# Kernel optimization log

Hardware: AMD Instinct MI355X
Metric: run time of the kernel (lower is better)

The kernel has to match this reference:

```python
import jax, jax.numpy as jnp
import numpy as np

B = 256      # batch
N_SRC = 10   # number of (x, y, mass) triplets per sample -> coord_v has 3*N_SRC cols
NMC = 16     # mass-channel bins
LL = 128     # spatial grid size


def setup_inputs() -> dict:
    key = jax.random.key(0)
    k1, = jax.random.split(key, 1)
    u = jax.random.uniform(k1, (B, 3 * N_SRC), dtype=jnp.float32)
    cols = jnp.arange(3 * N_SRC)
    is_mass = (cols % 3) == 2
    # x,y uniform in [0,1); mass = 10**(3u) in [1,1000) so log10(mass)/3 in [0,1)
    coord_v = jnp.where(is_mass, 10.0 ** (u * 3.0), u)
    lows = jnp.array([0.0, 0.0, 0.0], dtype=jnp.float32)
    highs = jnp.array([1.0, 1.0, 3.0], dtype=jnp.float32)
    return {"coord_v": coord_v, "lows": lows, "highs": highs, "nmc": NMC, "L": LL}


def reference(coord_v, lows, highs, nmc, L):
    n_batch, n_cols = coord_v.shape
    n = n_cols // 3  # number of triplets per sample

    # v_to_grid: log10 the mass columns, then normalize by tiled lows/highs
    v10 = coord_v.at[:, 2::3].set(jnp.log10(coord_v[:, 2::3]))
    lo = jnp.tile(lows, n)   # [3n]
    hi = jnp.tile(highs, n)  # [3n]
    coord_grid = (v10 - lo) / (hi - lo)  # [B, 3n]

    tr = coord_grid.reshape(-1, 3)  # [B*n, 3] rows of (x, y, m)
    x_i = jnp.floor(tr[:, 0] * L).astype(jnp.int32)
    y_i = jnp.floor(tr[:, 1] * L).astype(jnp.int32)
    m_i = jnp.floor(tr[:, 2] * nmc).astype(jnp.int32)
    b_i = jnp.repeat(jnp.arange(n_batch, dtype=jnp.int32), n)  # floor(arange(0,B,1/n))

    z = jnp.zeros((n_batch, nmc, L, L), dtype=coord_v.dtype)
    z = z.at[b_i, m_i, y_i, x_i].set(1.0)
    return jnp.concatenate((1.0 - z, z), axis=1)  # [B, 2*nmc, L, L]
```

## Files before the change

kernel.cpp:

```cpp
#include <hip/hip_runtime.h>
#include <hip/hip_bf16.h>
#include <math.h>

#define NSRC 10
#define NMC  16
#define LSZ  128
#define PLANE (LSZ * LSZ)

__device__ __forceinline__ float bf16f(unsigned short h) {
    union { unsigned int u; float f; } c;
    c.u = ((unsigned int)h) << 16;
    return c.f;
}

__device__ __forceinline__ float bf16r(float f) {
    union { float f; unsigned int u; } c;
    c.f = f;
    unsigned int lsb = (c.u >> 16) & 1u;
    c.u += 0x7FFFu + lsb;
    c.u &= 0xFFFF0000u;
    return c.f;
}

extern "C" __global__ __launch_bounds__(256)
void CustomParameterTransform_2491081031994_kernel(
    const void* __restrict__ coord_v,
    const void* __restrict__ pA,
    const void* __restrict__ pB,
    void* __restrict__ out_v)
{
    const int blk = blockIdx.x;
    const int b   = blk >> 4;
    const int m   = blk & (NMC - 1);

    const unsigned short* cu = (const unsigned short*)coord_v;
    bool isbf = true;
    #pragma unroll
    for (int j = 2; j < 3 * NSRC; j += 3) {
        float v = bf16f(cu[j]);
        if (!(v >= 0.5f && v <= 2048.0f)) isbf = false;
    }

    float a2, b2;
    if (isbf) {
        a2 = bf16f(((const unsigned short*)pA)[2]);
        b2 = bf16f(((const unsigned short*)pB)[2]);
    } else {
        a2 = ((const float*)pA)[2];
        b2 = ((const float*)pB)[2];
    }
    const void* lows_v  = (a2 < b2) ? pA : pB;
    const void* highs_v = (a2 < b2) ? pB : pA;

    __shared__ int s_pos[NSRC];
    __shared__ int s_cnt;
    if (threadIdx.x == 0) s_cnt = 0;
    __syncthreads();

    if (threadIdx.x < NSRC) {
        int xi, yi, mi;
        if (isbf) {
            const unsigned short* t = cu + b * (3 * NSRC) + threadIdx.x * 3;
            float x    = bf16f(t[0]);
            float y    = bf16f(t[1]);
            float mass = bf16f(t[2]);
            const unsigned short* lw = (const unsigned short*)lows_v;
            const unsigned short* hg = (const unsigned short*)highs_v;
            float lo0 = bf16f(lw[0]), lo1 = bf16f(lw[1]), lo2 = bf16f(lw[2]);
            float hi0 = bf16f(hg[0]), hi1 = bf16f(hg[1]), hi2 = bf16f(hg[2]);
            float d0 = bf16r(hi0 - lo0);
            float d1 = bf16r(hi1 - lo1);
            float d2 = bf16r(hi2 - lo2);
            float xg = bf16r(bf16r(x - lo0) / d0);
            float yg = bf16r(bf16r(y - lo1) / d1);
            float l10 = bf16r((float)log10((double)mass));
            float mg  = bf16r(bf16r(l10 - lo2) / d2);
            xi = (int)floorf(bf16r(xg * (float)LSZ));
            yi = (int)floorf(bf16r(yg * (float)LSZ));
            mi = (int)floorf(bf16r(mg * (float)NMC));
        } else {
            const float* cf = (const float*)coord_v;
            const float* t = cf + b * (3 * NSRC) + threadIdx.x * 3;
            const float* lw = (const float*)lows_v;
            const float* hg = (const float*)highs_v;
            float xg = (t[0] - lw[0]) / (hg[0] - lw[0]);
            float yg = (t[1] - lw[1]) / (hg[1] - lw[1]);
            float mg = ((float)log10((double)t[2]) - lw[2]) / (hg[2] - lw[2]);
            xi = (int)floorf(xg * (float)LSZ);
            yi = (int)floorf(yg * (float)LSZ);
            mi = (int)floorf(mg * (float)NMC);
        }
        if (mi == m && (unsigned)xi < (unsigned)LSZ && (unsigned)yi < (unsigned)LSZ) {
            int slot = atomicAdd(&s_cnt, 1);
            s_pos[slot] = yi * LSZ + xi;
        }
    }
    __syncthreads();
    const int cnt = s_cnt;

    if (isbf) {
        unsigned short* p0 = (unsigned short*)out_v + ((size_t)b * (2 * NMC) + m) * PLANE;
        unsigned short* p1 = p0 + (size_t)NMC * PLANE;
        for (int base = threadIdx.x * 8; base < PLANE; base += 256 * 8) {
            union { uint4 v; unsigned short s[8]; } z, o;
            z.v = make_uint4(0u, 0u, 0u, 0u);
            for (int j = 0; j < cnt; ++j) {
                int d = s_pos[j] - base;
                if (d >= 0 && d < 8) z.s[d] = 0x3F80;
            }
            #pragma unroll
            for (int k = 0; k < 8; ++k) o.s[k] = z.s[k] ? 0 : 0x3F80;
            *(uint4*)(p0 + base) = o.v;
            *(uint4*)(p1 + base) = z.v;
        }
    } else {
        float* p0 = (float*)out_v + ((size_t)b * (2 * NMC) + m) * PLANE;
        float* p1 = p0 + (size_t)NMC * PLANE;
        for (int base = threadIdx.x * 4; base < PLANE; base += 256 * 4) {
            float4 z = make_float4(0.f, 0.f, 0.f, 0.f);
            for (int j = 0; j < cnt; ++j) {
                int d = s_pos[j] - base;
                if (d >= 0 && d < 4) ((float*)&z)[d] = 1.0f;
            }
            float4 one = make_float4(1.f - z.x, 1.f - z.y, 1.f - z.z, 1.f - z.w);
            *(float4*)(p0 + base) = one;
            *(float4*)(p1 + base) = z;
        }
    }
}

static bool try_bind(const long* v, int n, int& ic, int& iA, int& iB, long& nbc) {
    for (int i = 0; i < n; ++i) if (v[i] < 1) return false;
    int lc = -1, a = -1, b = -1;
    for (int i = 0; i < n; ++i)
        if (v[i] >= 30 && v[i] % 30 == 0) { if (lc >= 0) return false; lc = i; }
    if (lc < 0) return false;
    for (int i = 0; i < n; ++i) {
        if (i == lc) continue;
        if (v[i] == 3) { if (a < 0) a = i; else if (b < 0) b = i; else return false; }
    }
    if (a < 0 || b < 0) return false;
    ic = lc; iA = a; iB = b; nbc = v[lc] / 30;
    return true;
}

extern "C" void kernel_launch(void* const* d_in, const int* in_sizes, int n_in,
                              void* d_out, int out_size, void* d_ws, size_t ws_size,
                              hipStream_t stream) {
    int ic = 0, iA = 1, iB = 2;
    long nbc = -1;
    const int n = (n_in > 8) ? 8 : (n_in > 0 ? n_in : 0);
    long v[8];
    bool ok = false;
    if (n >= 3) {
        for (int i = 0; i < n; ++i) v[i] = (long)in_sizes[i];
        ok = try_bind(v, n, ic, iA, iB, nbc);
        if (!ok) {
            const long long* s64 = (const long long*)in_sizes;
            for (int i = 0; i < n; ++i) v[i] = (long)s64[i];
            ok = try_bind(v, n, ic, iA, iB, nbc);
        }
        if (!ok) { ic = 0; iA = 1; iB = 2; nbc = -1; }
    }

    long nb_out = (out_size > 0) ? (long)out_size / (2L * NMC * PLANE) : -1;
    long nb = (nbc > 0) ? nbc : nb_out;
    if (nbc > 0 && nb_out > 0 && nb_out < nb) nb = nb_out;
    if (nb <= 0) nb = 1;

    dim3 grid((unsigned)(nb * NMC));
    dim3 block(256);
    CustomParameterTransform_2491081031994_kernel<<<grid, block, 0, stream>>>(
        d_in[ic], d_in[iA], d_in[iB], d_out);
}
```

Before: 538.2 us.

## Split into constant fill kernel plus sparse point scatter kernel

Replaces the per-plane kernel, which checked every output vector against the list of hits, with two kernels. The first writes constant one or zero planes, and the second has one thread per source point write the two affected cells. This removes the per-element loop over hit positions and the shared-memory atomics and barriers from the bandwidth-bound store loop. The cost is a second kernel launch and the ordering dependency between the two kernels.

```diff
diff --git a/kernel.cpp b/kernel.cpp
--- a/kernel.cpp
+++ b/kernel.cpp
@@ -6,6 +6,9 @@
 #define NMC  16
 #define LSZ  128
 #define PLANE (LSZ * LSZ)
+
+typedef unsigned int uintv4 __attribute__((ext_vector_type(4)));
+typedef float        fltv4  __attribute__((ext_vector_type(4)));
 
 __device__ __forceinline__ float bf16f(unsigned short h) {
     union { unsigned int u; float f; } c;
@@ -22,24 +25,53 @@
     return c.f;
 }
 
-extern "C" __global__ __launch_bounds__(256)
-void CustomParameterTransform_2491081031994_kernel(
-    const void* __restrict__ coord_v,
-    const void* __restrict__ pA,
-    const void* __restrict__ pB,
-    void* __restrict__ out_v)
-{
-    const int blk = blockIdx.x;
-    const int b   = blk >> 4;
-    const int m   = blk & (NMC - 1);
-
-    const unsigned short* cu = (const unsigned short*)coord_v;
+__device__ __forceinline__ bool detect_bf16(const unsigned short* cu) {
     bool isbf = true;
     #pragma unroll
     for (int j = 2; j < 3 * NSRC; j += 3) {
         float v = bf16f(cu[j]);
         if (!(v >= 0.5f && v <= 2048.0f)) isbf = false;
     }
+    return isbf;
+}
+
+extern "C" __global__ __launch_bounds__(256)
+void CustomParameterTransform_2491081031994_fill(
+    const void* __restrict__ coord_v,
+    void* __restrict__ out_v)
+{
+    const bool isbf = detect_bf16((const unsigned short*)coord_v);
+    const int pid = blockIdx.x;
+    const bool ones = (pid & 31) < 16;
+
+    if (isbf) {
+        unsigned short* p = (unsigned short*)out_v + (size_t)pid * PLANE;
+        const unsigned int w = ones ? 0x3F803F80u : 0u;
+        const uintv4 val = { w, w, w, w };
+        for (int base = threadIdx.x * 8; base < PLANE; base += 256 * 8)
+            *(uintv4*)(p + base) = val;
+    } else {
+        float* p = (float*)out_v + (size_t)pid * PLANE;
+        const float w = ones ? 1.0f : 0.0f;
+        const fltv4 val = { w, w, w, w };
+        for (int base = threadIdx.x * 4; base < PLANE; base += 256 * 4)
+            *(fltv4*)(p + base) = val;
+    }
+}
+
+extern "C" __global__ __launch_bounds__(256)
+void CustomParameterTransform_2491081031994_scatter(
+    const void* __restrict__ coord_v,
+    const void* __restrict__ pA,
+    const void* __restrict__ pB,
+    void* __restrict__ out_v,
+    int total)
+{
+    const int tid = blockIdx.x * 256 + threadIdx.x;
+    if (tid >= total) return;
+
+    const unsigned short* cu = (const unsigned short*)coord_v;
+    const bool isbf = detect_bf16(cu);
 
     float a2, b2;
     if (isbf) {
@@ -52,80 +84,54 @@
     const void* lows_v  = (a2 < b2) ? pA : pB;
     const void* highs_v = (a2 < b2) ? pB : pA;
 
-    __shared__ int s_pos[NSRC];
-    __shared__ int s_cnt;
-    if (threadIdx.x == 0) s_cnt = 0;
-    __syncthreads();
+    const int b = tid / NSRC;
+    const int s = tid - b * NSRC;
 
-    if (threadIdx.x < NSRC) {
-        int xi, yi, mi;
-        if (isbf) {
-            const unsigned short* t = cu + b * (3 * NSRC) + threadIdx.x * 3;
-            float x    = bf16f(t[0]);
-            float y    = bf16f(t[1]);
-            float mass = bf16f(t[2]);
-            const unsigned short* lw = (const unsigned short*)lows_v;
-            const unsigned short* hg = (const unsigned short*)highs_v;
-            float lo0 = bf16f(lw[0]), lo1 = bf16f(lw[1]), lo2 = bf16f(lw[2]);
-            float hi0 = bf16f(hg[0]), hi1 = bf16f(hg[1]), hi2 = bf16f(hg[2]);
-            float d0 = bf16r(hi0 - lo0);
-            float d1 = bf16r(hi1 - lo1);
-            float d2 = bf16r(hi2 - lo2);
-            float xg = bf16r(bf16r(x - lo0) / d0);
-            float yg = bf16r(bf16r(y - lo1) / d1);
-            float l10 = bf16r((float)log10((double)mass));
-            float mg  = bf16r(bf16r(l10 - lo2) / d2);
-            xi = (int)floorf(bf16r(xg * (float)LSZ));
-            yi = (int)floorf(bf16r(yg * (float)LSZ));
-            mi = (int)floorf(bf16r(mg * (float)NMC));
-        } else {
-            const float* cf = (const float*)coord_v;
-            const float* t = cf + b * (3 * NSRC) + threadIdx.x * 3;
-            const float* lw = (const float*)lows_v;
-            const float* hg = (const float*)highs_v;
-            float xg = (t[0] - lw[0]) / (hg[0] - lw[0]);
-            float yg = (t[1] - lw[1]) / (hg[1] - lw[1]);
-            float mg = ((float)log10((double)t[2]) - lw[2]) / (hg[2] - lw[2]);
-            xi = (int)floorf(xg * (float)LSZ);
-            yi = (int)floorf(yg * (float)LSZ);
-            mi = (int)floorf(mg * (float)NMC);
-        }
-        if (mi == m && (unsigned)xi < (unsigned)LSZ && (unsigned)yi < (unsigned)LSZ) {
-            int slot = atomicAdd(&s_cnt, 1);
-            s_pos[slot] = yi * LSZ + xi;
-        }
+    int xi, yi, mi;
+    if (isbf) {
+        const unsigned short* t = cu + b * (3 * NSRC) + s * 3;
+        float x    = bf16f(t[0]);
+        float y    = bf16f(t[1]);
+        float mass = bf16f(t[2]);
+        const unsigned short* lw = (const unsigned short*)lows_v;
+        const unsigned short* hg = (const unsigned short*)highs_v;
+        float lo0 = bf16f(lw[0]), lo1 = bf16f(lw[1]), lo2 = bf16f(lw[2]);
+        float hi0 = bf16f(hg[0]), hi1 = bf16f(hg[1]), hi2 = bf16f(hg[2]);
+        float d0 = bf16r(hi0 - lo0);
+        float d1 = bf16r(hi1 - lo1);
+        float d2 = bf16r(hi2 - lo2);
+        float xg = bf16r(bf16r(x - lo0) / d0);
+        float yg = bf16r(bf16r(y - lo1) / d1);
+        float l10 = bf16r((float)log10((double)mass));
+        float mg  = bf16r(bf16r(l10 - lo2) / d2);
+        xi = (int)floorf(bf16r(xg * (float)LSZ));
+        yi = (int)floorf(bf16r(yg * (float)LSZ));
+        mi = (int)floorf(bf16r(mg * (float)NMC));
+    } else {
+        const float* cf = (const float*)coord_v;
+        const float* t = cf + b * (3 * NSRC) + s * 3;
+        const float* lw = (const float*)lows_v;
+        const float* hg = (const float*)highs_v;
+        float xg = (t[0] - lw[0]) / (hg[0] - lw[0]);
+        float yg = (t[1] - lw[1]) / (hg[1] - lw[1]);
+        float mg = ((float)log10((double)t[2]) - lw[2]) / (hg[2] - lw[2]);
+        xi = (int)floorf(xg * (float)LSZ);
+        yi = (int)floorf(yg * (float)LSZ);
+        mi = (int)floorf(mg * (float)NMC);
     }
-    __syncthreads();
-    const int cnt = s_cnt;
+    if ((unsigned)mi >= (unsigned)NMC ||
+        (unsigned)xi >= (unsigned)LSZ ||
+        (unsigned)yi >= (unsigned)LSZ) return;
 
+    const size_t cell = ((size_t)b * (2 * NMC) + mi) * PLANE + yi * LSZ + xi;
     if (isbf) {
-        unsigned short* p0 = (unsigned short*)out_v + ((size_t)b * (2 * NMC) + m) * PLANE;
-        unsigned short* p1 = p0 + (size_t)NMC * PLANE;
-        for (int base = threadIdx.x * 8; base < PLANE; base += 256 * 8) {
-            union { uint4 v; unsigned short s[8]; } z, o;
-            z.v = make_uint4(0u, 0u, 0u, 0u);
-            for (int j = 0; j < cnt; ++j) {
-                int d = s_pos[j] - base;
-                if (d >= 0 && d < 8) z.s[d] = 0x3F80;
-            }
-            #pragma unroll
-            for (int k = 0; k < 8; ++k) o.s[k] = z.s[k] ? 0 : 0x3F80;
-            *(uint4*)(p0 + base) = o.v;
-            *(uint4*)(p1 + base) = z.v;
-        }
+        unsigned short* o = (unsigned short*)out_v;
+        o[cell] = 0;
+        o[cell + (size_t)NMC * PLANE] = 0x3F80;
     } else {
-        float* p0 = (float*)out_v + ((size_t)b * (2 * NMC) + m) * PLANE;
-        float* p1 = p0 + (size_t)NMC * PLANE;
-        for (int base = threadIdx.x * 4; base < PLANE; base += 256 * 4) {
-            float4 z = make_float4(0.f, 0.f, 0.f, 0.f);
-            for (int j = 0; j < cnt; ++j) {
-                int d = s_pos[j] - base;
-                if (d >= 0 && d < 4) ((float*)&z)[d] = 1.0f;
-            }
-            float4 one = make_float4(1.f - z.x, 1.f - z.y, 1.f - z.z, 1.f - z.w);
-            *(float4*)(p0 + base) = one;
-            *(float4*)(p1 + base) = z;
-        }
+        float* o = (float*)out_v;
+        o[cell] = 0.0f;
+        o[cell + (size_t)NMC * PLANE] = 1.0f;
     }
 }
 
@@ -168,8 +174,12 @@
     if (nbc > 0 && nb_out > 0 && nb_out < nb) nb = nb_out;
     if (nb <= 0) nb = 1;
 
-    dim3 grid((unsigned)(nb * NMC));
-    dim3 block(256);
-    CustomParameterTransform_2491081031994_kernel<<<grid, block, 0, stream>>>(
-        d_in[ic], d_in[iA], d_in[iB], d_out);
+    dim3 gfill((unsigned)(nb * 2 * NMC));
+    CustomParameterTransform_2491081031994_fill<<<gfill, dim3(256), 0, stream>>>(
+        d_in[ic], d_out);
+
+    int total = (int)(nb * NSRC);
+    dim3 gsc((unsigned)((total + 255) / 256));
+    CustomParameterTransform_2491081031994_scatter<<<gsc, dim3(256), 0, stream>>>(
+        d_in[ic], d_in[iA], d_in[iB], d_out, total);
 }
```

After: 535.6 us. About the same (-0.5%).
